# Performance work log

Hardware: AMD Instinct MI355X
Metric: run time of the kernel (lower is better)

Reference implementation:

```python
import jax, jax.numpy as jnp
import numpy as np

N_NODES = 100000
N_EDGES = 1600000
N_FEAT = 512
N_HID = 256
N_CLASS = 40


def setup_inputs() -> dict:
    key = jax.random.key(0)
    ks = jax.random.split(key, 6)
    features = jax.random.normal(ks[0], (N_NODES, N_FEAT), dtype=jnp.float32)
    edge_index = jax.random.randint(ks[1], (2, N_EDGES), 0, N_NODES, dtype=jnp.int32)
    edge_weight = jax.random.uniform(ks[2], (N_EDGES,), dtype=jnp.float32)
    # xavier_uniform with gain=1.414 (as in reset_parameters)
    g = 1.414
    lim1 = g * np.sqrt(6.0 / (N_FEAT + N_HID))
    lim2 = g * np.sqrt(6.0 / (N_HID + N_CLASS))
    W1 = jax.random.uniform(ks[3], (N_FEAT, N_HID), minval=-lim1, maxval=lim1, dtype=jnp.float32)
    W2 = jax.random.uniform(ks[4], (N_HID, N_CLASS), minval=-lim2, maxval=lim2, dtype=jnp.float32)
    b1 = jnp.zeros((N_HID,), dtype=jnp.float32)
    b2 = jnp.zeros((N_CLASS,), dtype=jnp.float32)
    return {"features": features, "edge_index": edge_index, "edge_weight": edge_weight,
            "W1": W1, "b1": b1, "W2": W2, "b2": b2}


def _spmm(edge_index, edge_weight, x, n):
    # out[r] = sum over edges e with row[e]==r of w[e] * x[col[e]]
    row, col = edge_index[0], edge_index[1]
    msgs = edge_weight[:, None] * x[col]  # [E, D]
    return jax.ops.segment_sum(msgs, row, num_segments=n)


def reference(features, edge_index, edge_weight, W1, b1, W2, b2):
    n = features.shape[0]
    # Layer 1: linear -> spmm -> relu (dropout is identity in eval mode)
    h = features @ W1 + b1
    h = jax.nn.relu(_spmm(edge_index, edge_weight, h, n))
    # Layer 2: linear -> spmm -> log_softmax
    h = h @ W2 + b2
    h = _spmm(edge_index, edge_weight, h, n)
    return jax.nn.log_softmax(h, axis=1)
```

## Files before the change

kernel.cpp:

```cpp
#include <hip/hip_runtime.h>
#include <stdint.h>

#define N_NODES 100000
#define N_EDGES 1600000
#define N_FEAT 512
#define N_HID 256
#define N_CLASS 40
#define H2SB 64

typedef float f32x4 __attribute__((ext_vector_type(4)));
typedef __bf16 bf16x8 __attribute__((ext_vector_type(8)));
typedef unsigned short u16x4 __attribute__((ext_vector_type(4)));
typedef unsigned short u16x8 __attribute__((ext_vector_type(8)));

__device__ __forceinline__ unsigned short f2bf(float f) {
  unsigned int u = __float_as_uint(f);
  unsigned int r = (u + 0x7FFFu + ((u >> 16) & 1u)) >> 16;
  return (unsigned short)r;
}
__device__ __forceinline__ float bf2f(unsigned short s) {
  return __uint_as_float(((unsigned int)s) << 16);
}
__device__ __forceinline__ float pk_w(unsigned int p) {
  return __uint_as_float((p >> 17) << 16);
}
__device__ __forceinline__ int pk_c(unsigned int p) { return (int)(p & 0x1FFFFu); }

__global__ __launch_bounds__(1024) void k_zero(int* __restrict__ cnt) {
  int i = blockIdx.x * 1024 + threadIdx.x;
  if (i < N_NODES) cnt[i] = 0;
}

#define HIST_BLOCKS 1563
#define W1T_BLOCKS  512
#define W2T_BLOCKS  48
__global__ __launch_bounds__(256) void k_pre(const float* __restrict__ W1,
                                             const float* __restrict__ W2,
                                             const int* __restrict__ ei,
                                             unsigned short* __restrict__ W1t,
                                             unsigned short* __restrict__ W2t,
                                             int* __restrict__ cnt,
                                             int* __restrict__ rank) {
  const int bid = blockIdx.x, tid = threadIdx.x;
  if (bid < HIST_BLOCKS) {
    #pragma unroll
    for (int k = 0; k < 4; ++k) {
      int e = bid * 1024 + k * 256 + tid;
      if (e < N_EDGES) rank[e] = atomicAdd(&cnt[ei[e]], 1);
    }
  } else if (bid < HIST_BLOCKS + W1T_BLOCKS) {
    int gid = (bid - HIST_BLOCKS) * 256 + tid;
    int n = gid >> 9, k = gid & 511;
    W1t[gid] = f2bf(W1[(long)k * N_HID + n]);
  } else {
    int gid = (bid - HIST_BLOCKS - W1T_BLOCKS) * 256 + tid;
    int n = gid >> 8, k = gid & 255;
    W2t[gid] = (n < N_CLASS) ? f2bf(W2[(long)k * N_CLASS + n]) : (unsigned short)0;
  }
}

__global__ __launch_bounds__(1024) void k_scan_a(const int* __restrict__ cnt,
                                                 int* __restrict__ rp,
                                                 int* __restrict__ bsum) {
  __shared__ int sm[1024];
  const int tid = threadIdx.x;
  const int i = blockIdx.x * 1024 + tid;
  int v = (i < N_NODES) ? cnt[i] : 0;
  sm[tid] = v;
  __syncthreads();
  #pragma unroll
  for (int d = 1; d < 1024; d <<= 1) {
    int t = (tid >= d) ? sm[tid - d] : 0;
    __syncthreads();
    sm[tid] += t;
    __syncthreads();
  }
  if (i < N_NODES) rp[i] = sm[tid] - v;
  if (tid == 1023) bsum[blockIdx.x] = sm[1023];
}

__global__ __launch_bounds__(128) void k_scan_b(const int* __restrict__ bsum,
                                                int* __restrict__ boffs,
                                                int* __restrict__ rp) {
  __shared__ int sm[128];
  const int tid = threadIdx.x;
  const int nb = (N_NODES + 1023) >> 10;
  int v = (tid < nb) ? bsum[tid] : 0;
  sm[tid] = v;
  __syncthreads();
  #pragma unroll
  for (int d = 1; d < 128; d <<= 1) {
    int t = (tid >= d) ? sm[tid - d] : 0;
    __syncthreads();
    sm[tid] += t;
    __syncthreads();
  }
  boffs[tid] = sm[tid] - v;
  if (tid == 127) rp[N_NODES] = sm[127];
}

__global__ void k_scan_c(int* __restrict__ rp, const int* __restrict__ boffs) {
  int i = blockIdx.x * 256 + threadIdx.x;
  if (i >= N_NODES) return;
  rp[i] += boffs[i >> 10];
}

__global__ __launch_bounds__(512) void k_scatter(const int* __restrict__ ei,
                                                 const float* __restrict__ ew,
                                                 const int* __restrict__ rank,
                                                 const int* __restrict__ rp,
                                                 unsigned int* __restrict__ cwp) {
  const int t = threadIdx.x;
  #pragma unroll
  for (int k = 0; k < 4; ++k) {
    int e = blockIdx.x * 2048 + k * 512 + t;
    if (e < N_EDGES) {
      int r = ei[e];
      int pos = rp[r] + rank[e];
      unsigned int w15 = (unsigned int)f2bf(ew[e]);
      cwp[pos] = (w15 << 17) | (unsigned int)ei[N_EDGES + e];
    }
  }
}

__global__ __launch_bounds__(1024) void k_gemm1(const float* __restrict__ X,
                                                const unsigned short* __restrict__ W1t,
                                                const float* __restrict__ b1,
                                                unsigned short* __restrict__ H1) {
  __shared__ __align__(16) unsigned short Bs[128 * 512];
  const int t = threadIdx.x;
  const int pair = blockIdx.x >> 1, panel = blockIdx.x & 1;
  const long rb = (long)pair * 800;
  const int n0 = panel * 128;

  {
    const int col = t >> 3, seg = t & 7;
    const unsigned short* src = W1t + (long)(n0 + col) * N_FEAT;
    #pragma unroll
    for (int j = 0; j < 8; ++j) {
      int slot = seg * 8 + j;
      int ps = slot ^ (col & 7);
      *(u16x8*)&Bs[col * 512 + ps * 8] = *(const u16x8*)(src + slot * 8);
    }
  }
  __syncthreads();

  const int lane = t & 63;
  const int wid = t >> 6;
  const int lr = lane & 15;
  const int lkg = lane >> 4;

  for (int c = wid; c < 50; c += 16) {
    const long row0 = rb + c * 16;
    const float* ap = X + (row0 + lr) * N_FEAT + lkg * 8;
    f32x4 acc[8] = {};

    #pragma unroll 2
    for (int k0 = 0; k0 < N_FEAT; k0 += 32) {
      f32x4 xa = *(const f32x4*)(ap + k0);
      f32x4 xb = *(const f32x4*)(ap + k0 + 4);
      bf16x8 av;
      av[0] = (__bf16)xa[0]; av[1] = (__bf16)xa[1];
      av[2] = (__bf16)xa[2]; av[3] = (__bf16)xa[3];
      av[4] = (__bf16)xb[0]; av[5] = (__bf16)xb[1];
      av[6] = (__bf16)xb[2]; av[7] = (__bf16)xb[3];
      const int slot = (k0 >> 3) + lkg;
      const int ps = slot ^ (lr & 7);
      #pragma unroll
      for (int nt = 0; nt < 8; ++nt) {
        bf16x8 bv = *(const bf16x8*)&Bs[(nt * 16 + lr) * 512 + ps * 8];
        acc[nt] = __builtin_amdgcn_mfma_f32_16x16x32_bf16(av, bv, acc[nt], 0, 0, 0);
      }
    }

    #pragma unroll
    for (int nt = 0; nt < 8; ++nt) {
      int colg = n0 + nt * 16 + lr;
      float bias = b1[colg];
      #pragma unroll
      for (int i = 0; i < 4; ++i) {
        long row = row0 + lkg * 4 + i;
        H1[row * N_HID + colg] = f2bf(acc[nt][i] + bias);
      }
    }
  }
}

__global__ __launch_bounds__(256) void k_spmm1(const int* __restrict__ row_ptr,
                                               const unsigned int* __restrict__ cwp,
                                               const unsigned short* __restrict__ H1,
                                               unsigned short* __restrict__ H1r) {
  int r = blockIdx.x * 4 + (threadIdx.x >> 6);
  int lane = threadIdx.x & 63;
  if (r >= N_NODES) return;
  int s = row_ptr[r], e = row_ptr[r + 1];
  float a0 = 0.f, a1 = 0.f, a2 = 0.f, a3 = 0.f;
  const unsigned short* Hb = H1 + lane * 4;
  int i = s;
  for (; i + 16 <= e; i += 16) {
    uint4 q0 = *(const uint4*)(cwp + i);
    uint4 q1 = *(const uint4*)(cwp + i + 4);
    uint4 q2 = *(const uint4*)(cwp + i + 8);
    uint4 q3 = *(const uint4*)(cwp + i + 12);
    unsigned int cc[16] = {q0.x, q0.y, q0.z, q0.w, q1.x, q1.y, q1.z, q1.w,
                           q2.x, q2.y, q2.z, q2.w, q3.x, q3.y, q3.z, q3.w};
    u16x4 h[16];
    #pragma unroll
    for (int j = 0; j < 16; ++j)
      h[j] = *(const u16x4*)(Hb + (long)pk_c(cc[j]) * N_HID);
    #pragma unroll
    for (int j = 0; j < 16; ++j) {
      float w = pk_w(cc[j]);
      a0 += w * bf2f(h[j][0]);
      a1 += w * bf2f(h[j][1]);
      a2 += w * bf2f(h[j][2]);
      a3 += w * bf2f(h[j][3]);
    }
  }
  for (; i + 4 <= e; i += 4) {
    uint4 q = *(const uint4*)(cwp + i);
    unsigned int cc[4] = {q.x, q.y, q.z, q.w};
    u16x4 h[4];
    #pragma unroll
    for (int j = 0; j < 4; ++j)
      h[j] = *(const u16x4*)(Hb + (long)pk_c(cc[j]) * N_HID);
    #pragma unroll
    for (int j = 0; j < 4; ++j) {
      float w = pk_w(cc[j]);
      a0 += w * bf2f(h[j][0]);
      a1 += w * bf2f(h[j][1]);
      a2 += w * bf2f(h[j][2]);
      a3 += w * bf2f(h[j][3]);
    }
  }
  for (; i < e; ++i) {
    unsigned int p = cwp[i];
    float w = pk_w(p);
    u16x4 hv = *(const u16x4*)(Hb + (long)pk_c(p) * N_HID);
    a0 += w * bf2f(hv[0]);
    a1 += w * bf2f(hv[1]);
    a2 += w * bf2f(hv[2]);
    a3 += w * bf2f(hv[3]);
  }
  u16x4 o;
  o[0] = f2bf(fmaxf(a0, 0.f));
  o[1] = f2bf(fmaxf(a1, 0.f));
  o[2] = f2bf(fmaxf(a2, 0.f));
  o[3] = f2bf(fmaxf(a3, 0.f));
  *(u16x4*)(H1r + (long)r * N_HID + lane * 4) = o;
}

__global__ __launch_bounds__(256) void k_gemm2(const unsigned short* __restrict__ H1r,
                                               const unsigned short* __restrict__ W2t,
                                               const float* __restrict__ b2,
                                               unsigned short* __restrict__ H2) {
  const int t = threadIdx.x;
  const int lane = t & 63;
  const int wid = t >> 6;
  const long m0 = (long)blockIdx.x * 128;
  const int lr = lane & 15;
  const int lk = (lane >> 4) * 8;

  const unsigned short* Ab[2];
  #pragma unroll
  for (int mt = 0; mt < 2; ++mt) {
    long r = m0 + wid * 32 + mt * 16 + lr;
    if (r >= N_NODES) r = N_NODES - 1;
    Ab[mt] = H1r + r * N_HID + lk;
  }
  const unsigned short* Bb[3];
  #pragma unroll
  for (int nt = 0; nt < 3; ++nt)
    Bb[nt] = W2t + (long)(nt * 16 + lr) * N_HID + lk;

  f32x4 acc[2][3] = {};
  #pragma unroll
  for (int k0 = 0; k0 < N_HID; k0 += 32) {
    bf16x8 av[2], bvv[3];
    #pragma unroll
    for (int mt = 0; mt < 2; ++mt) av[mt] = *(const bf16x8*)(Ab[mt] + k0);
    #pragma unroll
    for (int nt = 0; nt < 3; ++nt) bvv[nt] = *(const bf16x8*)(Bb[nt] + k0);
    #pragma unroll
    for (int mt = 0; mt < 2; ++mt)
      #pragma unroll
      for (int nt = 0; nt < 3; ++nt)
        acc[mt][nt] = __builtin_amdgcn_mfma_f32_16x16x32_bf16(av[mt], bvv[nt], acc[mt][nt], 0, 0, 0);
  }

  #pragma unroll
  for (int nt = 0; nt < 3; ++nt) {
    int col = nt * 16 + lr;
    if (col < N_CLASS) {
      float bias = b2[col];
      #pragma unroll
      for (int mt = 0; mt < 2; ++mt) {
        #pragma unroll
        for (int i = 0; i < 4; ++i) {
          long row = m0 + wid * 32 + mt * 16 + (lane >> 4) * 4 + i;
          if (row < N_NODES) H2[row * H2SB + col] = f2bf(acc[mt][nt][i] + bias);
        }
      }
    }
  }
}

__global__ __launch_bounds__(256) void k_spmm2_lsm(const int* __restrict__ row_ptr,
                                                   const unsigned int* __restrict__ cwp,
                                                   const unsigned short* __restrict__ H2,
                                                   float* __restrict__ out) {
  int r = blockIdx.x * 4 + (threadIdx.x >> 6);
  int lane = threadIdx.x & 63;
  if (r >= N_NODES) return;
  int s = row_ptr[r], e = row_ptr[r + 1];
  float acc = 0.f;
  const bool act = lane < N_CLASS;
  int i = s;
  for (; i + 8 <= e; i += 8) {
    uint4 q0 = *(const uint4*)(cwp + i);
    uint4 q1 = *(const uint4*)(cwp + i + 4);
    unsigned int cc[8] = {q0.x, q0.y, q0.z, q0.w, q1.x, q1.y, q1.z, q1.w};
    float h[8];
    #pragma unroll
    for (int j = 0; j < 8; ++j)
      h[j] = act ? bf2f(H2[(long)pk_c(cc[j]) * H2SB + lane]) : 0.f;
    #pragma unroll
    for (int j = 0; j < 8; ++j) acc += pk_w(cc[j]) * h[j];
  }
  for (; i < e; ++i) {
    unsigned int p = cwp[i];
    if (act) acc += pk_w(p) * bf2f(H2[(long)pk_c(p) * H2SB + lane]);
  }
  float v = act ? acc : -INFINITY;
  float m = v;
  #pragma unroll
  for (int d = 32; d > 0; d >>= 1) m = fmaxf(m, __shfl_xor(m, d));
  float ex = act ? __expf(v - m) : 0.f;
  float ssum = ex;
  #pragma unroll
  for (int d = 32; d > 0; d >>= 1) ssum += __shfl_xor(ssum, d);
  float ls = __logf(ssum);
  if (act) out[(long)r * N_CLASS + lane] = v - m - ls;
}

extern "C" void kernel_launch(void* const* d_in, const int* in_sizes, int n_in,
                              void* d_out, int out_size, void* d_ws, size_t ws_size,
                              hipStream_t stream) {
  (void)in_sizes; (void)n_in; (void)out_size; (void)ws_size;
  const float* X  = (const float*)d_in[0];
  const int*   EI = (const int*)d_in[1];
  const float* EW = (const float*)d_in[2];
  const float* W1 = (const float*)d_in[3];
  const float* b1 = (const float*)d_in[4];
  const float* W2 = (const float*)d_in[5];
  const float* b2 = (const float*)d_in[6];
  float* out = (float*)d_out;

  char* p = (char*)d_ws;
  auto take = [&](size_t bytes) {
    char* r = p;
    p += (bytes + 511) & ~(size_t)511;
    return r;
  };
  unsigned short* W1t   = (unsigned short*)take((size_t)N_HID * N_FEAT * 2);
  unsigned short* W2t   = (unsigned short*)take((size_t)48 * N_HID * 2);
  int*            cnt   = (int*)take((size_t)N_NODES * 4);
  int*            rp    = (int*)take((size_t)(N_NODES + 1) * 4);
  int*            bsum  = (int*)take((size_t)128 * 4);
  int*            boffs = (int*)take((size_t)128 * 4);
  int*            rank  = (int*)take((size_t)N_EDGES * 4);
  unsigned int*   cwp   = (unsigned int*)take((size_t)N_EDGES * 4);
  unsigned short* H1    = (unsigned short*)take((size_t)N_NODES * N_HID * 2);
  unsigned short* H1r   = (unsigned short*)take((size_t)N_NODES * N_HID * 2);
  unsigned short* H2    = (unsigned short*)take((size_t)N_NODES * H2SB * 2);

  const int NB_SCAN = (N_NODES + 1023) / 1024;

  k_zero<<<NB_SCAN, 1024, 0, stream>>>(cnt);
  k_pre<<<HIST_BLOCKS + W1T_BLOCKS + W2T_BLOCKS, 256, 0, stream>>>(W1, W2, EI, W1t, W2t, cnt, rank);
  k_scan_a<<<NB_SCAN, 1024, 0, stream>>>(cnt, rp, bsum);
  k_scan_b<<<1, 128, 0, stream>>>(bsum, boffs, rp);
  k_scan_c<<<(N_NODES + 255) / 256, 256, 0, stream>>>(rp, boffs);
  k_scatter<<<(N_EDGES + 2047) / 2048, 512, 0, stream>>>(EI, EW, rank, rp, cwp);
  k_gemm1<<<250, 1024, 0, stream>>>(X, W1t, b1, H1);
  k_spmm1<<<(N_NODES + 3) / 4, 256, 0, stream>>>(rp, cwp, H1, H1r);
  k_gemm2<<<(N_NODES + 127) / 128, 256, 0, stream>>>(H1r, W2t, b2, H2);
  k_spmm2_lsm<<<(N_NODES + 3) / 4, 256, 0, stream>>>(rp, cwp, H2, out);
}
```

Before: 466.3 us.

## Fuse edge scatter into GEMM1 launch, use nontemporal X loads, shrink SpMM unroll

Merges the CSR scatter kernel and the first GEMM into one launch, with extra blocks doing the scatter so the two independent stages can run concurrently. X loads in the GEMM become nontemporal to avoid polluting cache with streamed data. The SpMM1 inner loop unroll drops from 16+4 to 8, cutting register pressure at the cost of less memory-level parallelism. Scatter blocks still allocate the 128KB shared array, which limits their occupancy.

```diff
diff --git a/kernel.cpp b/kernel.cpp
--- a/kernel.cpp
+++ b/kernel.cpp
@@ -105,30 +105,35 @@
   rp[i] += boffs[i >> 10];
 }
 
-__global__ __launch_bounds__(512) void k_scatter(const int* __restrict__ ei,
+#define GEMM_BLOCKS 250
+#define SCAT_BLOCKS 782
+__global__ __launch_bounds__(1024) void k_fused1(const float* __restrict__ X,
+                                                 const unsigned short* __restrict__ W1t,
+                                                 const float* __restrict__ b1,
+                                                 unsigned short* __restrict__ H1,
+                                                 const int* __restrict__ ei,
                                                  const float* __restrict__ ew,
                                                  const int* __restrict__ rank,
                                                  const int* __restrict__ rp,
                                                  unsigned int* __restrict__ cwp) {
-  const int t = threadIdx.x;
-  #pragma unroll
-  for (int k = 0; k < 4; ++k) {
-    int e = blockIdx.x * 2048 + k * 512 + t;
-    if (e < N_EDGES) {
-      int r = ei[e];
-      int pos = rp[r] + rank[e];
-      unsigned int w15 = (unsigned int)f2bf(ew[e]);
-      cwp[pos] = (w15 << 17) | (unsigned int)ei[N_EDGES + e];
-    }
-  }
-}
-
-__global__ __launch_bounds__(1024) void k_gemm1(const float* __restrict__ X,
-                                                const unsigned short* __restrict__ W1t,
-                                                const float* __restrict__ b1,
-                                                unsigned short* __restrict__ H1) {
   __shared__ __align__(16) unsigned short Bs[128 * 512];
   const int t = threadIdx.x;
+
+  if (blockIdx.x >= GEMM_BLOCKS) {
+    int sb = blockIdx.x - GEMM_BLOCKS;
+    #pragma unroll
+    for (int k = 0; k < 2; ++k) {
+      int e = sb * 2048 + k * 1024 + t;
+      if (e < N_EDGES) {
+        int r = ei[e];
+        int pos = rp[r] + rank[e];
+        unsigned int w15 = (unsigned int)f2bf(ew[e]);
+        cwp[pos] = (w15 << 17) | (unsigned int)ei[N_EDGES + e];
+      }
+    }
+    return;
+  }
+
   const int pair = blockIdx.x >> 1, panel = blockIdx.x & 1;
   const long rb = (long)pair * 800;
   const int n0 = panel * 128;
@@ -157,8 +162,8 @@
 
     #pragma unroll 2
     for (int k0 = 0; k0 < N_FEAT; k0 += 32) {
-      f32x4 xa = *(const f32x4*)(ap + k0);
-      f32x4 xb = *(const f32x4*)(ap + k0 + 4);
+      f32x4 xa = __builtin_nontemporal_load((const f32x4*)(ap + k0));
+      f32x4 xb = __builtin_nontemporal_load((const f32x4*)(ap + k0 + 4));
       bf16x8 av;
       av[0] = (__bf16)xa[0]; av[1] = (__bf16)xa[1];
       av[2] = (__bf16)xa[2]; av[3] = (__bf16)xa[3];
@@ -197,35 +202,16 @@
   float a0 = 0.f, a1 = 0.f, a2 = 0.f, a3 = 0.f;
   const unsigned short* Hb = H1 + lane * 4;
   int i = s;
-  for (; i + 16 <= e; i += 16) {
+  for (; i + 8 <= e; i += 8) {
     uint4 q0 = *(const uint4*)(cwp + i);
     uint4 q1 = *(const uint4*)(cwp + i + 4);
-    uint4 q2 = *(const uint4*)(cwp + i + 8);
-    uint4 q3 = *(const uint4*)(cwp + i + 12);
-    unsigned int cc[16] = {q0.x, q0.y, q0.z, q0.w, q1.x, q1.y, q1.z, q1.w,
-                           q2.x, q2.y, q2.z, q2.w, q3.x, q3.y, q3.z, q3.w};
-    u16x4 h[16];
-    #pragma unroll
-    for (int j = 0; j < 16; ++j)
+    unsigned int cc[8] = {q0.x, q0.y, q0.z, q0.w, q1.x, q1.y, q1.z, q1.w};
+    u16x4 h[8];
+    #pragma unroll
+    for (int j = 0; j < 8; ++j)
       h[j] = *(const u16x4*)(Hb + (long)pk_c(cc[j]) * N_HID);
     #pragma unroll
-    for (int j = 0; j < 16; ++j) {
-      float w = pk_w(cc[j]);
-      a0 += w * bf2f(h[j][0]);
-      a1 += w * bf2f(h[j][1]);
-      a2 += w * bf2f(h[j][2]);
-      a3 += w * bf2f(h[j][3]);
-    }
-  }
-  for (; i + 4 <= e; i += 4) {
-    uint4 q = *(const uint4*)(cwp + i);
-    unsigned int cc[4] = {q.x, q.y, q.z, q.w};
-    u16x4 h[4];
-    #pragma unroll
-    for (int j = 0; j < 4; ++j)
-      h[j] = *(const u16x4*)(Hb + (long)pk_c(cc[j]) * N_HID);
-    #pragma unroll
-    for (int j = 0; j < 4; ++j) {
+    for (int j = 0; j < 8; ++j) {
       float w = pk_w(cc[j]);
       a0 += w * bf2f(h[j][0]);
       a1 += w * bf2f(h[j][1]);
@@ -381,8 +367,7 @@
   k_scan_a<<<NB_SCAN, 1024, 0, stream>>>(cnt, rp, bsum);
   k_scan_b<<<1, 128, 0, stream>>>(bsum, boffs, rp);
   k_scan_c<<<(N_NODES + 255) / 256, 256, 0, stream>>>(rp, boffs);
-  k_scatter<<<(N_EDGES + 2047) / 2048, 512, 0, stream>>>(EI, EW, rank, rp, cwp);
-  k_gemm1<<<250, 1024, 0, stream>>>(X, W1t, b1, H1);
+  k_fused1<<<GEMM_BLOCKS + SCAT_BLOCKS, 1024, 0, stream>>>(X, W1t, b1, H1, EI, EW, rank, rp, cwp);
   k_spmm1<<<(N_NODES + 3) / 4, 256, 0, stream>>>(rp, cwp, H1, H1r);
   k_gemm2<<<(N_NODES + 127) / 128, 256, 0, stream>>>(H1r, W2t, b2, H2);
   k_spmm2_lsm<<<(N_NODES + 3) / 4, 256, 0, stream>>>(rp, cwp, H2, out);
```

After: 476.6 us. 1.02x slower.
